# Kernel optimization log

Measured on AMD Instinct MI355X. Metric: run time of the kernel, lower is better.

The kernel has to match this reference:

```python
import jax, jax.numpy as jnp
import numpy as np

BSZ, IN_DIM, OUT_DIM = 512, 1024, 2048
M_AND = 5        # Anderson memory (self.m)
BETA = 1.0
LAM = 1e-4
ALPHA = 1.0
TOL = 1e-5
MAX_ITER = 50
M_MON = 1.0      # monotonicity parameter of MONSingleFc


def _multiply(A, B, z):
    # MONSingleFc.multiply: (1-m)z - z A^T A + z B^T - z B
    Az = z @ A.T
    return (1.0 - M_MON) * z - Az @ A + z @ B.T - z @ B


def _relu(z):
    return jnp.maximum(z, 0.0)


def _single_it(A, B, z, bias):
    zn = _multiply(A, B, z)
    zn = (1.0 - ALPHA) * z + ALPHA * (zn + bias)
    zn = _relu(zn)
    err = jnp.linalg.norm(zn - z) / (1e-6 + jnp.linalg.norm(zn))
    return zn, err


def _anderson_solve(A, B, bias):
    bsz, d = bias.shape
    dt = bias.dtype
    Z = jnp.zeros((bsz, M_AND, d), dt)
    F = jnp.zeros((bsz, M_AND, d), dt)
    z0 = jnp.zeros((bsz, d), dt)
    f0, _ = _single_it(A, B, z0, bias)
    F = F.at[:, 0].set(f0)
    Z = Z.at[:, 1].set(f0)
    f1, _ = _single_it(A, B, f0, bias)
    F = F.at[:, 1].set(f1)
    eye = jnp.eye(M_AND, dtype=dt)

    def cond(s):
        Z, F, it, err = s
        return (it < MAX_ITER) & (err > TOL)

    def body(s):
        Z, F, it, _ = s
        n = jnp.minimum(M_AND, it)
        mask = jnp.arange(M_AND) < n                         # active Anderson slots
        # For it < m the unused slots of Z and F are still zero, so G = F - Z
        # has zero rows there and GGt's Frobenius norm matches the :n slice.
        G = F - Z                                            # (bsz, m, d)
        GGt = jnp.einsum('bmd,bnd->bmn', G, G)
        nrm = jnp.linalg.norm(GGt.reshape(GGt.shape[0], -1), axis=-1)
        GGt = GGt / (nrm[:, None, None] + 1e-6)
        pair = mask[:, None] & mask[None, :]
        # identity padding on inactive slots keeps the solve well-posed and
        # yields alpha = 0 there, equivalent to slicing [:n+1, :n+1].
        Hb = jnp.where(pair, GGt + LAM * eye, eye)
        mk = mask.astype(dt)
        H = jnp.zeros((bsz, M_AND + 1, M_AND + 1), dt)
        H = H.at[:, 0, 1:].set(mk).at[:, 1:, 0].set(mk).at[:, 1:, 1:].set(Hb)
        y = jnp.zeros((bsz, M_AND + 1, 1), dt).at[:, 0, 0].set(1.0)
        alpha = jnp.linalg.solve(H, y)[:, 1:, 0]             # (bsz, m)
        z_new = BETA * jnp.einsum('bm,bmd->bd', alpha, F) \
              + (1.0 - BETA) * jnp.einsum('bm,bmd->bd', alpha, Z)
        slot = it % M_AND
        Z = Z.at[:, slot].set(z_new)
        zo, err = _single_it(A, B, z_new, bias)
        F = F.at[:, slot].set(zo)
        return Z, F, it + 1, err

    Z, F, it, err = jax.lax.while_loop(
        cond, body, (Z, F, jnp.array(2, jnp.int32), jnp.array(jnp.inf, dt)))
    slot = (it - 1) % M_AND
    return Z[:, slot]


def setup_inputs():
    key = jax.random.key(0)
    kx, ka, kb, kw, kub = jax.random.split(key, 5)
    s = 1.0 / np.sqrt(OUT_DIM).astype(np.float32)
    x = jax.random.normal(kx, (BSZ, IN_DIM), jnp.float32)
    # scaled so ||W|| < 1 -> forward-backward splitting converges (trained MON regime)
    A = 0.3 * s * jax.random.normal(ka, (OUT_DIM, OUT_DIM), jnp.float32)
    B = 0.1 * s * jax.random.normal(kb, (OUT_DIM, OUT_DIM), jnp.float32)
    U_W = (1.0 / np.sqrt(IN_DIM).astype(np.float32)) * jax.random.normal(kw, (OUT_DIM, IN_DIM), jnp.float32)
    U_b = 0.01 * jax.random.normal(kub, (OUT_DIM,), jnp.float32)
    return {"x": x, "A": A, "B": B, "U_W": U_W, "U_b": U_b}


def reference(x, A, B, U_W, U_b):
    bias = x @ U_W.T + U_b                       # linear_module.bias(x)
    z_star = _anderson_solve(A, B, bias)         # equilibrium (no-grad in torch)
    zn = _relu(_multiply(A, B, z_star) + bias)   # final full step: nonlin(linear(x, z*))
    return zn
```

## Files before the change

### kernel.cpp

```cpp
#include <hip/hip_runtime.h>
#include <hip/hip_bf16.h>
#include <math.h>

#define BSZ      512
#define IN_DIM   1024
#define OUT_DIM  2048
#define M_AND    5
#define LAM      1e-4f
#define TOL      1e-5f
#define MAX_ITER 50
#define SPLIT_IT 16
#define NBLK     256
#define ITERBLK  512

typedef __bf16 bf16x8 __attribute__((ext_vector_type(8)));
typedef float  f32x4  __attribute__((ext_vector_type(4)));
typedef unsigned short u16x8 __attribute__((ext_vector_type(8)));
typedef unsigned short u16x4 __attribute__((ext_vector_type(4)));
typedef __hip_bfloat16 bf16;

#define GAS __attribute__((address_space(1)))
#define LAS __attribute__((address_space(3)))

#define S_WAITCNT_VMCNT(N) asm volatile("s_waitcnt vmcnt(" #N ")" ::: "memory")

union BU { bf16 b; unsigned short u; };

__device__ __forceinline__ float bf2f(unsigned short u) {
    union { unsigned int i; float f; } c; c.i = (unsigned int)u << 16; return c.f;
}
__device__ __forceinline__ unsigned short f2bf(float f) {
    BU t; t.b = __float2bfloat16(f); return t.u;
}

static constexpr size_t BIAS_B = 0;
static constexpr size_t F_B    = BIAS_B + (size_t)BSZ * OUT_DIM * 4;
static constexpr size_t G_B    = F_B    + (size_t)BSZ * M_AND * OUT_DIM * 4;
static constexpr size_t ZH_B   = G_B    + (size_t)BSZ * M_AND * OUT_DIM * 2;
static constexpr size_t ZL_B   = ZH_B   + (size_t)BSZ * OUT_DIM * 2;
static constexpr size_t XH_B   = ZL_B   + (size_t)BSZ * OUT_DIM * 2;
static constexpr size_t XL_B   = XH_B   + (size_t)BSZ * IN_DIM * 2;
static constexpr size_t UH_B   = XL_B   + (size_t)BSZ * IN_DIM * 2;
static constexpr size_t UL_B   = UH_B   + (size_t)OUT_DIM * IN_DIM * 2;
static constexpr size_t AT_B   = UL_B   + (size_t)OUT_DIM * IN_DIM * 2;
static constexpr size_t WT_B   = AT_B   + (size_t)OUT_DIM * OUT_DIM * 2;
static constexpr size_t RED_B  = WT_B   + (size_t)OUT_DIM * OUT_DIM * 2;
static constexpr size_t BAR_B  = RED_B  + 512;
static constexpr size_t CTR_B  = BAR_B  + 64;
static constexpr size_t FLAG_B = CTR_B  + 256;
static constexpr size_t FSLOT_B = FLAG_B + 16;
static constexpr size_t CTRL_SZ = 512 + 64 + 256 + 16 + 16;

template<int ROUNDS>
__device__ __forceinline__ void stage_tile(const void* __restrict__ g0, int row_bytes,
                                           void* l0, int tid)
{
    #pragma unroll
    for (int q = 0; q < ROUNDS; ++q) {
        const int D   = q * 4096 + tid * 16;
        const int r   = D >> 7;
        const int cb  = D & 127;
        const int scb = cb ^ ((r & 7) << 4);
        const char* gsrc = (const char*)g0 + (size_t)r * row_bytes + scb;
        char* ldst = (char*)l0 + q * 4096 + (tid >> 6) * 1024;
        __builtin_amdgcn_global_load_lds((const GAS void*)gsrc, (LAS void*)ldst, 16, 0, 0);
    }
}

__device__ __forceinline__ bf16x8 read_frag(const void* tile, int row, int cb)
{
    return *(const bf16x8*)((const char*)tile + row * 128 + (cb ^ ((row & 7) << 4)));
}

__device__ __forceinline__ void gsync(unsigned int* bar)
{
    __syncthreads();
    if (threadIdx.x == 0) {
        __threadfence();
        const unsigned int g =
            __hip_atomic_load(&bar[1], __ATOMIC_ACQUIRE, __HIP_MEMORY_SCOPE_AGENT);
        const unsigned int a =
            __hip_atomic_fetch_add(&bar[0], 1u, __ATOMIC_ACQ_REL, __HIP_MEMORY_SCOPE_AGENT);
        if (a == NBLK - 1) {
            __hip_atomic_store(&bar[0], 0u, __ATOMIC_RELAXED, __HIP_MEMORY_SCOPE_AGENT);
            __hip_atomic_fetch_add(&bar[1], 1u, __ATOMIC_RELEASE, __HIP_MEMORY_SCOPE_AGENT);
        } else {
            while (__hip_atomic_load(&bar[1], __ATOMIC_ACQUIRE, __HIP_MEMORY_SCOPE_AGENT) == g)
                __builtin_amdgcn_s_sleep(1);
        }
        __threadfence();
    }
    __syncthreads();
}

__global__ __launch_bounds__(256)
void conv_hilo(const float* __restrict__ src, bf16* __restrict__ h, bf16* __restrict__ l)
{
    const size_t i4 = ((size_t)blockIdx.x * 256 + threadIdx.x) * 4;
    const float4 v = *(const float4*)&src[i4];
    const float vv[4] = {v.x, v.y, v.z, v.w};
    union { short4 s4; unsigned short u[4]; } ph, pl;
    #pragma unroll
    for (int j = 0; j < 4; ++j) {
        ph.u[j] = f2bf(vv[j]);
        pl.u[j] = f2bf(vv[j] - bf2f(ph.u[j]));
    }
    *(short4*)((char*)h + i4 * 2) = ph.s4;
    *(short4*)((char*)l + i4 * 2) = pl.s4;
}

__global__ __launch_bounds__(256)
void prep_at(const float* __restrict__ A, bf16* __restrict__ At)
{
    __shared__ float t[64][65];
    const int tid = threadIdx.x;
    const int k0 = blockIdx.y * 64, c0 = blockIdx.x * 64;
    const int cc = tid & 63, rr = tid >> 6;
    #pragma unroll
    for (int q = 0; q < 16; ++q)
        t[rr + 4 * q][cc] = A[(size_t)(k0 + rr + 4 * q) * OUT_DIM + c0 + cc];
    __syncthreads();
    #pragma unroll
    for (int q = 0; q < 16; ++q)
        At[(size_t)(c0 + rr + 4 * q) * OUT_DIM + k0 + cc] = __float2bfloat16(t[cc][rr + 4 * q]);
}

__global__ __launch_bounds__(256)
void w_mfma(const bf16* __restrict__ At, const float* __restrict__ Bm, bf16* __restrict__ Wt)
{
    __shared__ __align__(16) bf16 lds[2][2][64 * 64];
    const int tid = threadIdx.x;
    const int lane = tid & 63, wid = tid >> 6;
    const int wy = wid >> 1, wx = wid & 1;

    int bb = blockIdx.x;
    int ti = (int)((sqrtf(8.f * bb + 1.f) - 1.f) * 0.5f);
    while ((ti + 1) * (ti + 2) / 2 <= bb) ++ti;
    while (ti * (ti + 1) / 2 > bb) --ti;
    const int tj = bb - ti * (ti + 1) / 2;
    const int r0 = ti * 64, c0 = tj * 64;
    const bool diag = (ti == tj);

    f32x4 acc[2][2];
    #pragma unroll
    for (int i = 0; i < 2; ++i)
        #pragma unroll
        for (int j = 0; j < 2; ++j) acc[i][j] = 0;

    stage_tile<2>(At + (size_t)r0 * OUT_DIM, OUT_DIM * 2, lds[0][0], tid);
    stage_tile<2>(At + (size_t)c0 * OUT_DIM, OUT_DIM * 2, lds[0][1], tid);
    __syncthreads();
    int cur = 0;
    for (int t = 0; t < 32; ++t) {
        if (t + 1 < 32) {
            const int kk = (t + 1) * 64;
            stage_tile<2>(At + (size_t)r0 * OUT_DIM + kk, OUT_DIM * 2, lds[cur ^ 1][0], tid);
            stage_tile<2>(At + (size_t)c0 * OUT_DIM + kk, OUT_DIM * 2, lds[cur ^ 1][1], tid);
        }
        const bf16* Ta = lds[cur][0];
        const bf16* Tb = lds[cur][1];
        #pragma unroll
        for (int kf = 0; kf < 2; ++kf) {
            const int cb = kf * 64 + (lane >> 4) * 16;
            bf16x8 bfr[2];
            #pragma unroll
            for (int nj = 0; nj < 2; ++nj)
                bfr[nj] = read_frag(Tb, wx * 32 + nj * 16 + (lane & 15), cb);
            #pragma unroll
            for (int mi = 0; mi < 2; ++mi) {
                bf16x8 afr = read_frag(Ta, wy * 32 + mi * 16 + (lane & 15), cb);
                #pragma unroll
                for (int nj = 0; nj < 2; ++nj)
                    acc[mi][nj] = __builtin_amdgcn_mfma_f32_16x16x32_bf16(afr, bfr[nj], acc[mi][nj], 0, 0, 0);
            }
        }
        __syncthreads();
        cur ^= 1;
    }

    #pragma unroll
    for (int mi = 0; mi < 2; ++mi) {
        const int rb = r0 + wy * 32 + mi * 16 + (lane >> 4) * 4;
        #pragma unroll
        for (int nj = 0; nj < 2; ++nj) {
            const int c = c0 + wx * 32 + nj * 16 + (lane & 15);
            const float4 bc = *(const float4*)&Bm[(size_t)c * OUT_DIM + rb];
            const float bcv[4] = {bc.x, bc.y, bc.z, bc.w};
            union { short4 s4; unsigned short u[4]; } p;
            #pragma unroll
            for (int g = 0; g < 4; ++g) {
                const float a = acc[mi][nj][g];
                const float brc = Bm[(size_t)(rb + g) * OUT_DIM + c];
                const float w = bcv[g] - brc - a;
                p.u[g] = f2bf(w);
                if (!diag) {
                    const float wm = brc - bcv[g] - a;
                    *((unsigned short*)Wt + (size_t)(rb + g) * OUT_DIM + c) = f2bf(wm);
                }
            }
            *(short4*)((char*)Wt + ((size_t)c * OUT_DIM + rb) * 2) = p.s4;
        }
    }
}

__global__ __launch_bounds__(256)
void bias_mfma(const bf16* __restrict__ xh, const bf16* __restrict__ xl,
               const bf16* __restrict__ uh, const bf16* __restrict__ ul,
               const float* __restrict__ Ub, float* __restrict__ bias,
               float* __restrict__ F, unsigned short* __restrict__ G,
               unsigned short* __restrict__ zh, unsigned short* __restrict__ zl)
{
    __shared__ __align__(16) bf16 lds[2][4][64 * 64];
    const int tid = threadIdx.x;
    const int lane = tid & 63, wid = tid >> 6;
    const int wy = wid >> 1, wx = wid & 1;
    const int m0 = blockIdx.y * 64, n0 = blockIdx.x * 64;

    f32x4 acc[2][2];
    #pragma unroll
    for (int i = 0; i < 2; ++i)
        #pragma unroll
        for (int j = 0; j < 2; ++j) acc[i][j] = 0;

    stage_tile<2>(xh + (size_t)m0 * IN_DIM, IN_DIM * 2, lds[0][0], tid);
    stage_tile<2>(xl + (size_t)m0 * IN_DIM, IN_DIM * 2, lds[0][1], tid);
    stage_tile<2>(uh + (size_t)n0 * IN_DIM, IN_DIM * 2, lds[0][2], tid);
    stage_tile<2>(ul + (size_t)n0 * IN_DIM, IN_DIM * 2, lds[0][3], tid);
    __syncthreads();
    int cur = 0;
    for (int t = 0; t < 16; ++t) {
        if (t + 1 < 16) {
            const int kk = (t + 1) * 64;
            stage_tile<2>(xh + (size_t)m0 * IN_DIM + kk, IN_DIM * 2, lds[cur ^ 1][0], tid);
            stage_tile<2>(xl + (size_t)m0 * IN_DIM + kk, IN_DIM * 2, lds[cur ^ 1][1], tid);
            stage_tile<2>(uh + (size_t)n0 * IN_DIM + kk, IN_DIM * 2, lds[cur ^ 1][2], tid);
            stage_tile<2>(ul + (size_t)n0 * IN_DIM + kk, IN_DIM * 2, lds[cur ^ 1][3], tid);
        }
        const bf16* Txh = lds[cur][0];
        const bf16* Txl = lds[cur][1];
        const bf16* Tuh = lds[cur][2];
        const bf16* Tul = lds[cur][3];
        #pragma unroll
        for (int kf = 0; kf < 2; ++kf) {
            const int cb = kf * 64 + (lane >> 4) * 16;
            bf16x8 bh[2], bl[2];
            #pragma unroll
            for (int nj = 0; nj < 2; ++nj) {
                const int br = wx * 32 + nj * 16 + (lane & 15);
                bh[nj] = read_frag(Tuh, br, cb);
                bl[nj] = read_frag(Tul, br, cb);
            }
            #pragma unroll
            for (int mi = 0; mi < 2; ++mi) {
                const int ar = wy * 32 + mi * 16 + (lane & 15);
                bf16x8 ah = read_frag(Txh, ar, cb);
                bf16x8 al = read_frag(Txl, ar, cb);
                #pragma unroll
                for (int nj = 0; nj < 2; ++nj) {
                    acc[mi][nj] = __builtin_amdgcn_mfma_f32_16x16x32_bf16(ah, bh[nj], acc[mi][nj], 0, 0, 0);
                    acc[mi][nj] = __builtin_amdgcn_mfma_f32_16x16x32_bf16(ah, bl[nj], acc[mi][nj], 0, 0, 0);
                    acc[mi][nj] = __builtin_amdgcn_mfma_f32_16x16x32_bf16(al, bh[nj], acc[mi][nj], 0, 0, 0);
                }
            }
        }
        __syncthreads();
        cur ^= 1;
    }

    #pragma unroll
    for (int mi = 0; mi < 2; ++mi) {
        const int mb = m0 + wy * 32 + mi * 16 + (lane >> 4) * 4;
        #pragma unroll
        for (int nj = 0; nj < 2; ++nj) {
            const int n = n0 + wx * 32 + nj * 16 + (lane & 15);
            const float ub = Ub[n];
            #pragma unroll
            for (int g = 0; g < 4; ++g) {
                const int m = mb + g;
                const size_t idx = (size_t)m * OUT_DIM + n;
                const float v = acc[mi][nj][g] + ub;
                bias[idx] = v;
                const float f = fmaxf(v, 0.f);
                F[((size_t)m * M_AND + 0) * OUT_DIM + n] = f;
                G[((size_t)m * M_AND + 0) * OUT_DIM + n] = f2bf(f);
                const unsigned short h = f2bf(f);
                zh[idx] = h;
                zl[idx] = f2bf(f - bf2f(h));
            }
        }
    }
}

template<bool DO_ERR>
__device__ __forceinline__ void iter_core(
    const int m0, const int n0, const int tid,
    const unsigned short* __restrict__ zh, const unsigned short* __restrict__ zl,
    const bf16* __restrict__ Wt, const float* __restrict__ bias,
    float* __restrict__ F, unsigned short* __restrict__ G,
    float* red, bf16* lds_buf, const int slot, const int it)
{
    const int lane = tid & 63, wid = tid >> 6;
    const int wy = wid >> 1, wx = wid & 1;

    const int Dz  = tid * 16;
    const int zr  = Dz >> 7,  zcb  = Dz & 127;
    const size_t z_ro = (size_t)zr * 4096 + zcb;
    const int zo_l = zr * 128 + (zcb ^ ((zr & 7) << 4));
    const int Dw1 = 4096 + tid * 16;
    const int wr0 = Dz >> 7,  wcb0 = Dz & 127;
    const int wr1 = Dw1 >> 7, wcb1 = Dw1 & 127;
    const size_t w_ro0 = (size_t)wr0 * 4096 + wcb0;
    const size_t w_ro1 = (size_t)wr1 * 4096 + wcb1;
    const int wo_l0 = wr0 * 128 + (wcb0 ^ ((wr0 & 7) << 4));
    const int wo_l1 = wr1 * 128 + (wcb1 ^ ((wr1 & 7) << 4));

    const char* zbase = (const char*)zh + (size_t)m0 * 4096;
    const char* lbase = (const char*)zl + (size_t)m0 * 4096;
    const char* wbase = (const char*)Wt + (size_t)n0 * 4096;

    f32x4 acc[2];
    acc[0] = 0; acc[1] = 0;

    float4 rza, rla, rw0a, rw1a, rzb, rlb, rw0b, rw1b;

#define LOADR_(RZ, RL, RW0, RW1, KK)                                         \
    RZ  = *(const float4*)(zbase + (size_t)(KK) * 2 + z_ro);                 \
    RL  = *(const float4*)(lbase + (size_t)(KK) * 2 + z_ro);                 \
    RW0 = *(const float4*)(wbase + (size_t)(KK) * 2 + w_ro0);                \
    RW1 = *(const float4*)(wbase + (size_t)(KK) * 2 + w_ro1);

#define STEP_(T, RZ, RL, RW0, RW1, CUR)                                      \
  {                                                                          \
    if ((T) + 1 < 32) { S_WAITCNT_VMCNT(4); } else { S_WAITCNT_VMCNT(0); }   \
    __builtin_amdgcn_s_barrier();          \
    char* bp = (char*)lds_buf + (CUR) * 16384;                               \
    *(float4*)(bp + zo_l)         = RZ;                                      \
    *(float4*)(bp + 4096 + zo_l)  = RL;                                      \
    *(float4*)(bp + 8192 + wo_l0) = RW0;                                     \
    *(float4*)(bp + 8192 + wo_l1) = RW1;                                     \
    if ((T) + 2 < 32) { LOADR_(RZ, RL, RW0, RW1, ((T) + 2) * 64); }          \
    asm volatile("s_waitcnt lgkmcnt(0)" ::: "memory");                       \
    __builtin_amdgcn_sched_barrier(0);                                       \
    __builtin_amdgcn_s_barrier();         \
    __builtin_amdgcn_sched_barrier(0);                                       \
    __builtin_amdgcn_s_setprio(1);                                           \
    _Pragma("unroll")                                                        \
    for (int kf = 0; kf < 2; ++kf) {                                         \
        const int cb2 = kf * 64 + (lane >> 4) * 16;                          \
        bf16x8 b0  = read_frag(bp + 8192, wx * 32 + (lane & 15), cb2);       \
        bf16x8 b1  = read_frag(bp + 8192, wx * 32 + 16 + (lane & 15), cb2);  \
        bf16x8 ahv = read_frag(bp,        wy * 16 + (lane & 15), cb2);       \
        bf16x8 alv = read_frag(bp + 4096, wy * 16 + (lane & 15), cb2);       \
        acc[0] = __builtin_amdgcn_mfma_f32_16x16x32_bf16(ahv, b0, acc[0], 0, 0, 0); \
        acc[0] = __builtin_amdgcn_mfma_f32_16x16x32_bf16(alv, b0, acc[0], 0, 0, 0); \
        acc[1] = __builtin_amdgcn_mfma_f32_16x16x32_bf16(ahv, b1, acc[1], 0, 0, 0); \
        acc[1] = __builtin_amdgcn_mfma_f32_16x16x32_bf16(alv, b1, acc[1], 0, 0, 0); \
    }                                                                        \
    __builtin_amdgcn_s_setprio(0);                                           \
  }

    LOADR_(rza, rla, rw0a, rw1a, 0);
    LOADR_(rzb, rlb, rw0b, rw1b, 64);
    for (int tb = 0; tb < 16; ++tb) {
        const int t0 = 2 * tb;
        STEP_(t0,     rza, rla, rw0a, rw1a, 0);
        STEP_(t0 + 1, rzb, rlb, rw0b, rw1b, 1);
    }
#undef STEP_
#undef LOADR_

    float lnum = 0.f, lden = 0.f;
    const int mb = m0 + wy * 16 + (lane >> 4) * 4;
    #pragma unroll
    for (int nj = 0; nj < 2; ++nj) {
        const int n = n0 + wx * 32 + nj * 16 + (lane & 15);
        #pragma unroll
        for (int g = 0; g < 4; ++g) {
            const int m = mb + g;
            const size_t idx = (size_t)m * OUT_DIM + n;
            float v = acc[nj][g] + bias[idx];
            v = fmaxf(v, 0.f);
            const float zc = bf2f(zh[idx]) + bf2f(zl[idx]);
            const float gg = v - zc;
            F[((size_t)m * M_AND + slot) * OUT_DIM + n] = v;
            G[((size_t)m * M_AND + slot) * OUT_DIM + n] = f2bf(gg);
            if (DO_ERR) { lnum += gg * gg; lden += v * v; }
        }
    }

    if (DO_ERR) {
        #pragma unroll
        for (int off = 32; off; off >>= 1) {
            lnum += __shfl_down(lnum, off);
            lden += __shfl_down(lden, off);
        }
        __shared__ float swn[4], swd[4];
        if ((tid & 63) == 0) { swn[tid >> 6] = lnum; swd[tid >> 6] = lden; }
        __syncthreads();
        if (tid == 0) {
            atomicAdd(&red[2 * it],     swn[0] + swn[1] + swn[2] + swn[3]);
            atomicAdd(&red[2 * it + 1], swd[0] + swd[1] + swd[2] + swd[3]);
        }
    }
}

__device__ __forceinline__ void swz_mn(int bid, int& m0, int& n0)
{
    const int xcd = bid & 7, sl = bid >> 3;
    n0 = (xcd * 4 + (sl & 3)) * 64;
    m0 = (sl >> 2) * 32;
}

template<bool DO_ERR>
__global__ __launch_bounds__(256, 2)
void iter_mfma(const unsigned short* __restrict__ zh, const unsigned short* __restrict__ zl,
               const bf16* __restrict__ Wt, const float* __restrict__ bias,
               float* __restrict__ F, unsigned short* __restrict__ G,
               float* red, unsigned int* ctr, int* flag, int* fslot, int slot, int it)
{
    if (((volatile int*)flag)[0]) return;
    __shared__ __align__(16) bf16 lds_buf[2 * 8192];
    int m0, n0;
    swz_mn(blockIdx.x, m0, n0);
    iter_core<DO_ERR>(m0, n0, threadIdx.x, zh, zl, Wt, bias, F, G, red, lds_buf, slot, it);
    if (DO_ERR && threadIdx.x == 0) {
        __threadfence();
        const unsigned int done = atomicAdd(&ctr[it], 1u);
        if (done == ITERBLK - 1) {
            ((volatile int*)fslot)[0] = slot;
            const float num2 = ((volatile float*)red)[2 * it];
            const float den2 = ((volatile float*)red)[2 * it + 1];
            if (sqrtf(num2) <= TOL * (1e-6f + sqrtf(den2)))
                ((volatile int*)flag)[0] = 1;
        }
    }
}

__global__ __launch_bounds__(256)
void final_copy(const float* __restrict__ F, const int* __restrict__ fslot,
                float* __restrict__ out)
{
    const int s = ((volatile const int*)fslot)[0];
    const size_t i4 = ((size_t)blockIdx.x * 256 + threadIdx.x) * 4;
    const int m = (int)(i4 >> 11), n = (int)(i4 & 2047);
    *(float4*)&out[i4] = *(const float4*)&F[((size_t)m * M_AND + s) * OUT_DIM + n];
}

__global__ __launch_bounds__(512)
void anderson_kernel(const float* __restrict__ F, const unsigned short* __restrict__ G,
                     unsigned short* __restrict__ zh, unsigned short* __restrict__ zl,
                     int* flag, int it)
{
    if (((volatile int*)flag)[0]) return;
    const int b = blockIdx.x;
    const int tid = threadIdx.x;
    const int lane = tid & 63, wid = tid >> 6;
    const int n = (it < M_AND) ? it : M_AND;
    const int c0 = tid * 4;
    const unsigned short* Gb = G + (size_t)b * M_AND * OUT_DIM;
    const float* Fb = F + (size_t)b * M_AND * OUT_DIM;

    float g[M_AND][4];
    float4 f[M_AND];
    #pragma unroll
    for (int m = 0; m < M_AND; ++m) {
        f[m] = *(const float4*)(Fb + (size_t)m * OUT_DIM + c0);
        if (m < n) {
            const u16x4 gv = *(const u16x4*)(Gb + (size_t)m * OUT_DIM + c0);
            #pragma unroll
            for (int q = 0; q < 4; ++q) g[m][q] = bf2f(gv[q]);
        } else {
            #pragma unroll
            for (int q = 0; q < 4; ++q) g[m][q] = 0.f;
        }
    }

    float dots[15];
    {
        int p = 0;
        #pragma unroll
        for (int i = 0; i < M_AND; ++i)
            #pragma unroll
            for (int j = i; j < M_AND; ++j) {
                float s = 0.f;
                #pragma unroll
                for (int q = 0; q < 4; ++q) s += g[i][q] * g[j][q];
                dots[p++] = s;
            }
    }

    __shared__ float sred[15][8];
    #pragma unroll
    for (int p = 0; p < 15; ++p) {
        float v = dots[p];
        #pragma unroll
        for (int off = 32; off; off >>= 1) v += __shfl_xor(v, off);
        if (lane == 0) sred[p][wid] = v;
    }
    __syncthreads();

    __shared__ float s_alpha[M_AND];
    if (tid == 0) {
        float GGm[M_AND][M_AND];
        int p = 0;
        for (int i = 0; i < M_AND; ++i)
            for (int j = i; j < M_AND; ++j) {
                float v = 0.f;
                for (int w = 0; w < 8; ++w) v += sred[p][w];
                GGm[i][j] = v; GGm[j][i] = v; ++p;
            }
        float fro = 0.f;
        for (int i = 0; i < M_AND; ++i)
            for (int j = 0; j < M_AND; ++j) fro += GGm[i][j] * GGm[i][j];
        const float inv = 1.f / (sqrtf(fro) + 1e-6f);

        float Mm[M_AND][M_AND];
        for (int i = 0; i < n; ++i)
            for (int j = 0; j < n; ++j)
                Mm[i][j] = GGm[i][j] * inv + (i == j ? LAM : 0.f);

        float L[M_AND][M_AND];
        for (int i = 0; i < n; ++i)
            for (int j = 0; j <= i; ++j) {
                float s = Mm[i][j];
                for (int k = 0; k < j; ++k) s -= L[i][k] * L[j][k];
                L[i][j] = (i == j) ? sqrtf(fmaxf(s, 1e-20f)) : s / L[j][j];
            }
        float y[M_AND], u[M_AND];
        for (int i = 0; i < n; ++i) {
            float s = 1.f;
            for (int k = 0; k < i; ++k) s -= L[i][k] * y[k];
            y[i] = s / L[i][i];
        }
        for (int i = n - 1; i >= 0; --i) {
            float s = y[i];
            for (int k = i + 1; k < n; ++k) s -= L[k][i] * u[k];
            u[i] = s / L[i][i];
        }
        float su = 0.f;
        for (int i = 0; i < n; ++i) su += u[i];
        const float isu = 1.f / su;
        for (int m = 0; m < M_AND; ++m) s_alpha[m] = (m < n) ? u[m] * isu : 0.f;
    }
    __syncthreads();

    float z[4] = {};
    #pragma unroll
    for (int m = 0; m < M_AND; ++m) {
        if (m < n) {
            const float a = s_alpha[m];
            z[0] += a * f[m].x; z[1] += a * f[m].y;
            z[2] += a * f[m].z; z[3] += a * f[m].w;
        }
    }
    u16x4 hv, lv;
    #pragma unroll
    for (int q = 0; q < 4; ++q) {
        const unsigned short h = f2bf(z[q]);
        hv[q] = h;
        lv[q] = f2bf(z[q] - bf2f(h));
    }
    *(u16x4*)(zh + (size_t)b * OUT_DIM + c0) = hv;
    *(u16x4*)(zl + (size_t)b * OUT_DIM + c0) = lv;
}

__global__ __launch_bounds__(256)
void tail_loop(unsigned short* zh, unsigned short* zl,
               const bf16* __restrict__ Wt, const float* __restrict__ bias,
               float* F, unsigned short* G,
               float* red, unsigned int* bar, int* flag, int* fslot)
{
    if (((volatile int*)flag)[0]) return;
    __shared__ __align__(16) bf16 lds_buf[2 * 8192];
    __shared__ float sred2[2][2][15];
    __shared__ float s_alpha[2][M_AND];
    const int bid = blockIdx.x, tid = threadIdx.x;
    int m0a, n0a, m0b, n0b;
    swz_mn(bid, m0a, n0a);
    swz_mn(bid + 256, m0b, n0b);

    for (int it = SPLIT_IT; it < MAX_ITER; ++it) {
        {
            const int half = tid >> 7, lt = tid & 127;
            const int r = bid * 2 + half;
            const int wv = lt >> 6;
            const unsigned short* Gb = G + (size_t)r * M_AND * OUT_DIM;
            const float* Fb = F + (size_t)r * M_AND * OUT_DIM;
            const int c0 = lt * 16;

            float g[M_AND][16];
            #pragma unroll
            for (int m = 0; m < M_AND; ++m) {
                const u16x8 ga = *(const u16x8*)(Gb + (size_t)m * OUT_DIM + c0);
                const u16x8 gb2 = *(const u16x8*)(Gb + (size_t)m * OUT_DIM + c0 + 8);
                #pragma unroll
                for (int q = 0; q < 8; ++q) { g[m][q] = bf2f(ga[q]); g[m][8 + q] = bf2f(gb2[q]); }
            }
            {
                int p = 0;
                #pragma unroll
                for (int i = 0; i < M_AND; ++i)
                    #pragma unroll
                    for (int j = i; j < M_AND; ++j) {
                        float s = 0.f;
                        #pragma unroll
                        for (int q = 0; q < 16; ++q) s += g[i][q] * g[j][q];
                        float v = s;
                        #pragma unroll
                        for (int off = 32; off; off >>= 1) v += __shfl_xor(v, off);
                        if ((lt & 63) == 0) sred2[half][wv][p] = v;
                        ++p;
                    }
            }
            __syncthreads();
            if (lt == 0) {
                float GGm[M_AND][M_AND];
                int p = 0;
                for (int i = 0; i < M_AND; ++i)
                    for (int j = i; j < M_AND; ++j) {
                        const float v = sred2[half][0][p] + sred2[half][1][p];
                        GGm[i][j] = v; GGm[j][i] = v; ++p;
                    }
                float fro = 0.f;
                for (int i = 0; i < M_AND; ++i)
                    for (int j = 0; j < M_AND; ++j) fro += GGm[i][j] * GGm[i][j];
                const float inv = 1.f / (sqrtf(fro) + 1e-6f);
                float Mm[M_AND][M_AND];
                for (int i = 0; i < M_AND; ++i)
                    for (int j = 0; j < M_AND; ++j)
                        Mm[i][j] = GGm[i][j] * inv + (i == j ? LAM : 0.f);
                float L[M_AND][M_AND];
                for (int i = 0; i < M_AND; ++i)
                    for (int j = 0; j <= i; ++j) {
                        float s = Mm[i][j];
                        for (int k = 0; k < j; ++k) s -= L[i][k] * L[j][k];
                        L[i][j] = (i == j) ? sqrtf(fmaxf(s, 1e-20f)) : s / L[j][j];
                    }
                float y[M_AND], u[M_AND];
                for (int i = 0; i < M_AND; ++i) {
                    float s = 1.f;
                    for (int k = 0; k < i; ++k) s -= L[i][k] * y[k];
                    y[i] = s / L[i][i];
                }
                for (int i = M_AND - 1; i >= 0; --i) {
                    float s = y[i];
                    for (int k = i + 1; k < M_AND; ++k) s -= L[k][i] * u[k];
                    u[i] = s / L[i][i];
                }
                float su = 0.f;
                for (int i = 0; i < M_AND; ++i) su += u[i];
                const float isu = 1.f / su;
                for (int m = 0; m < M_AND; ++m) s_alpha[half][m] = u[m] * isu;
            }
            __syncthreads();
            float z[16] = {};
            for (int m = 0; m < M_AND; ++m) {
                const float a = s_alpha[half][m];
                #pragma unroll
                for (int q = 0; q < 4; ++q) {
                    const float4 fv = *(const float4*)(Fb + (size_t)m * OUT_DIM + c0 + q * 4);
                    z[q * 4 + 0] += a * fv.x; z[q * 4 + 1] += a * fv.y;
                    z[q * 4 + 2] += a * fv.z; z[q * 4 + 3] += a * fv.w;
                }
            }
            u16x8 hv[2], lv[2];
            #pragma unroll
            for (int q = 0; q < 16; ++q) {
                const unsigned short h = f2bf(z[q]);
                hv[q >> 3][q & 7] = h;
                lv[q >> 3][q & 7] = f2bf(z[q] - bf2f(h));
            }
            const size_t base = (size_t)r * OUT_DIM + c0;
            *(u16x8*)(zh + base)     = hv[0];
            *(u16x8*)(zh + base + 8) = hv[1];
            *(u16x8*)(zl + base)     = lv[0];
            *(u16x8*)(zl + base + 8) = lv[1];
        }
        gsync(bar);
        iter_core<true>(m0a, n0a, tid, zh, zl, Wt, bias, F, G, red, lds_buf, it % M_AND, it);
        __syncthreads();
        iter_core<true>(m0b, n0b, tid, zh, zl, Wt, bias, F, G, red, lds_buf, it % M_AND, it);
        gsync(bar);
        if (bid == 0 && tid == 0) ((volatile int*)fslot)[0] = it % M_AND;
        const float num2 = __hip_atomic_load(&red[2 * it], __ATOMIC_RELAXED, __HIP_MEMORY_SCOPE_AGENT);
        const float den2 = __hip_atomic_load(&red[2 * it + 1], __ATOMIC_RELAXED, __HIP_MEMORY_SCOPE_AGENT);
        if (sqrtf(num2) <= TOL * (1e-6f + sqrtf(den2))) break;
    }
}

extern "C" void kernel_launch(void* const* d_in, const int* in_sizes, int n_in,
                              void* d_out, int out_size, void* d_ws, size_t ws_size,
                              hipStream_t stream)
{
    const float* x  = (const float*)d_in[0];
    const float* A  = (const float*)d_in[1];
    const float* B  = (const float*)d_in[2];
    const float* UW = (const float*)d_in[3];
    const float* Ub = (const float*)d_in[4];
    float* out = (float*)d_out;
    char*  wsb = (char*)d_ws;

    float*          bias = (float*)(wsb + BIAS_B);
    float*          F    = (float*)(wsb + F_B);
    unsigned short* G    = (unsigned short*)(wsb + G_B);
    unsigned short* zh   = (unsigned short*)(wsb + ZH_B);
    unsigned short* zl   = (unsigned short*)(wsb + ZL_B);
    bf16*           xh   = (bf16*)(wsb + XH_B);
    bf16*           xl   = (bf16*)(wsb + XL_B);
    bf16*           uh   = (bf16*)(wsb + UH_B);
    bf16*           ul   = (bf16*)(wsb + UL_B);
    bf16*           At   = (bf16*)(wsb + AT_B);
    bf16*           Wt   = (bf16*)(wsb + WT_B);
    float*          red  = (float*)(wsb + RED_B);
    unsigned int*   bar  = (unsigned int*)(wsb + BAR_B);
    unsigned int*   ctr  = (unsigned int*)(wsb + CTR_B);
    int*            flag = (int*)(wsb + FLAG_B);
    int*            fslot= (int*)(wsb + FSLOT_B);

    hipMemsetAsync(wsb + RED_B, 0, CTRL_SZ, stream);

    conv_hilo<<<dim3(BSZ * IN_DIM / 1024),     256, 0, stream>>>(x,  xh, xl);
    conv_hilo<<<dim3(OUT_DIM * IN_DIM / 1024), 256, 0, stream>>>(UW, uh, ul);
    prep_at  <<<dim3(32, 32), 256, 0, stream>>>(A, At);
    w_mfma   <<<dim3(528), 256, 0, stream>>>(At, B, Wt);
    bias_mfma<<<dim3(32, 8), 256, 0, stream>>>(xh, xl, uh, ul, Ub, bias, F, G, zh, zl);

    iter_mfma<false><<<dim3(ITERBLK), 256, 0, stream>>>(zh, zl, Wt, bias, F, G,
                                                        red, ctr, flag, fslot, 1, 0);

    for (int it = 2; it < SPLIT_IT; ++it) {
        anderson_kernel<<<dim3(BSZ), 512, 0, stream>>>(F, G, zh, zl, flag, it);
        iter_mfma<true><<<dim3(ITERBLK), 256, 0, stream>>>(zh, zl, Wt, bias, F, G,
                                                           red, ctr, flag, fslot, it % M_AND, it);
    }
    tail_loop<<<dim3(NBLK), 256, 0, stream>>>(zh, zl, Wt, bias, F, G, red, bar, flag, fslot);
    final_copy<<<dim3(BSZ * OUT_DIM / 1024), 256, 0, stream>>>(F, fslot, out);
}
```

Measured before the change: 527.5 us.

## Fuse all Anderson iterations into one persistent 512-block kernel

The separate per-iteration anderson_kernel and iter_mfma launches for the first 16 iterations are removed. A single persistent kernel, solve_all, now runs with 512 blocks and grid barriers for every iteration. Each block handles one batch row's Anderson mixing and one GEMM tile per iteration, instead of the old tail loop's 256 blocks doing two tiles each. This removes about 28 kernel launches and the flag polling. In exchange it depends on all 512 blocks being co-resident, which launch_bounds(256,2) is meant to guarantee, and adds two grid barriers per iteration.

```diff
diff --git a/kernel.cpp b/kernel.cpp
--- a/kernel.cpp
+++ b/kernel.cpp
@@ -9,9 +9,7 @@
 #define LAM      1e-4f
 #define TOL      1e-5f
 #define MAX_ITER 50
-#define SPLIT_IT 16
-#define NBLK     256
-#define ITERBLK  512
+#define GS_N     512
 
 typedef __bf16 bf16x8 __attribute__((ext_vector_type(8)));
 typedef float  f32x4  __attribute__((ext_vector_type(4)));
@@ -46,10 +44,8 @@
 static constexpr size_t WT_B   = AT_B   + (size_t)OUT_DIM * OUT_DIM * 2;
 static constexpr size_t RED_B  = WT_B   + (size_t)OUT_DIM * OUT_DIM * 2;
 static constexpr size_t BAR_B  = RED_B  + 512;
-static constexpr size_t CTR_B  = BAR_B  + 64;
-static constexpr size_t FLAG_B = CTR_B  + 256;
-static constexpr size_t FSLOT_B = FLAG_B + 16;
-static constexpr size_t CTRL_SZ = 512 + 64 + 256 + 16 + 16;
+static constexpr size_t FSLOT_B = BAR_B + 64;
+static constexpr size_t CTRL_SZ = 512 + 64 + 16;
 
 template<int ROUNDS>
 __device__ __forceinline__ void stage_tile(const void* __restrict__ g0, int row_bytes,
@@ -81,7 +77,7 @@
             __hip_atomic_load(&bar[1], __ATOMIC_ACQUIRE, __HIP_MEMORY_SCOPE_AGENT);
         const unsigned int a =
             __hip_atomic_fetch_add(&bar[0], 1u, __ATOMIC_ACQ_REL, __HIP_MEMORY_SCOPE_AGENT);
-        if (a == NBLK - 1) {
+        if (a == GS_N - 1) {
             __hip_atomic_store(&bar[0], 0u, __ATOMIC_RELAXED, __HIP_MEMORY_SCOPE_AGENT);
             __hip_atomic_fetch_add(&bar[1], 1u, __ATOMIC_RELEASE, __HIP_MEMORY_SCOPE_AGENT);
         } else {
@@ -411,190 +407,41 @@
     m0 = (sl >> 2) * 32;
 }
 
-template<bool DO_ERR>
 __global__ __launch_bounds__(256, 2)
-void iter_mfma(const unsigned short* __restrict__ zh, const unsigned short* __restrict__ zl,
-               const bf16* __restrict__ Wt, const float* __restrict__ bias,
-               float* __restrict__ F, unsigned short* __restrict__ G,
-               float* red, unsigned int* ctr, int* flag, int* fslot, int slot, int it)
-{
-    if (((volatile int*)flag)[0]) return;
-    __shared__ __align__(16) bf16 lds_buf[2 * 8192];
-    int m0, n0;
-    swz_mn(blockIdx.x, m0, n0);
-    iter_core<DO_ERR>(m0, n0, threadIdx.x, zh, zl, Wt, bias, F, G, red, lds_buf, slot, it);
-    if (DO_ERR && threadIdx.x == 0) {
-        __threadfence();
-        const unsigned int done = atomicAdd(&ctr[it], 1u);
-        if (done == ITERBLK - 1) {
-            ((volatile int*)fslot)[0] = slot;
-            const float num2 = ((volatile float*)red)[2 * it];
-            const float den2 = ((volatile float*)red)[2 * it + 1];
-            if (sqrtf(num2) <= TOL * (1e-6f + sqrtf(den2)))
-                ((volatile int*)flag)[0] = 1;
-        }
-    }
-}
-
-__global__ __launch_bounds__(256)
-void final_copy(const float* __restrict__ F, const int* __restrict__ fslot,
-                float* __restrict__ out)
-{
-    const int s = ((volatile const int*)fslot)[0];
-    const size_t i4 = ((size_t)blockIdx.x * 256 + threadIdx.x) * 4;
-    const int m = (int)(i4 >> 11), n = (int)(i4 & 2047);
-    *(float4*)&out[i4] = *(const float4*)&F[((size_t)m * M_AND + s) * OUT_DIM + n];
-}
-
-__global__ __launch_bounds__(512)
-void anderson_kernel(const float* __restrict__ F, const unsigned short* __restrict__ G,
-                     unsigned short* __restrict__ zh, unsigned short* __restrict__ zl,
-                     int* flag, int it)
-{
-    if (((volatile int*)flag)[0]) return;
-    const int b = blockIdx.x;
-    const int tid = threadIdx.x;
-    const int lane = tid & 63, wid = tid >> 6;
-    const int n = (it < M_AND) ? it : M_AND;
-    const int c0 = tid * 4;
-    const unsigned short* Gb = G + (size_t)b * M_AND * OUT_DIM;
-    const float* Fb = F + (size_t)b * M_AND * OUT_DIM;
-
-    float g[M_AND][4];
-    float4 f[M_AND];
-    #pragma unroll
-    for (int m = 0; m < M_AND; ++m) {
-        f[m] = *(const float4*)(Fb + (size_t)m * OUT_DIM + c0);
-        if (m < n) {
-            const u16x4 gv = *(const u16x4*)(Gb + (size_t)m * OUT_DIM + c0);
-            #pragma unroll
-            for (int q = 0; q < 4; ++q) g[m][q] = bf2f(gv[q]);
-        } else {
-            #pragma unroll
-            for (int q = 0; q < 4; ++q) g[m][q] = 0.f;
-        }
-    }
-
-    float dots[15];
-    {
-        int p = 0;
-        #pragma unroll
-        for (int i = 0; i < M_AND; ++i)
-            #pragma unroll
-            for (int j = i; j < M_AND; ++j) {
-                float s = 0.f;
-                #pragma unroll
-                for (int q = 0; q < 4; ++q) s += g[i][q] * g[j][q];
-                dots[p++] = s;
-            }
-    }
-
-    __shared__ float sred[15][8];
-    #pragma unroll
-    for (int p = 0; p < 15; ++p) {
-        float v = dots[p];
-        #pragma unroll
-        for (int off = 32; off; off >>= 1) v += __shfl_xor(v, off);
-        if (lane == 0) sred[p][wid] = v;
-    }
-    __syncthreads();
-
-    __shared__ float s_alpha[M_AND];
-    if (tid == 0) {
-        float GGm[M_AND][M_AND];
-        int p = 0;
-        for (int i = 0; i < M_AND; ++i)
-            for (int j = i; j < M_AND; ++j) {
-                float v = 0.f;
-                for (int w = 0; w < 8; ++w) v += sred[p][w];
-                GGm[i][j] = v; GGm[j][i] = v; ++p;
-            }
-        float fro = 0.f;
-        for (int i = 0; i < M_AND; ++i)
-            for (int j = 0; j < M_AND; ++j) fro += GGm[i][j] * GGm[i][j];
-        const float inv = 1.f / (sqrtf(fro) + 1e-6f);
-
-        float Mm[M_AND][M_AND];
-        for (int i = 0; i < n; ++i)
-            for (int j = 0; j < n; ++j)
-                Mm[i][j] = GGm[i][j] * inv + (i == j ? LAM : 0.f);
-
-        float L[M_AND][M_AND];
-        for (int i = 0; i < n; ++i)
-            for (int j = 0; j <= i; ++j) {
-                float s = Mm[i][j];
-                for (int k = 0; k < j; ++k) s -= L[i][k] * L[j][k];
-                L[i][j] = (i == j) ? sqrtf(fmaxf(s, 1e-20f)) : s / L[j][j];
-            }
-        float y[M_AND], u[M_AND];
-        for (int i = 0; i < n; ++i) {
-            float s = 1.f;
-            for (int k = 0; k < i; ++k) s -= L[i][k] * y[k];
-            y[i] = s / L[i][i];
-        }
-        for (int i = n - 1; i >= 0; --i) {
-            float s = y[i];
-            for (int k = i + 1; k < n; ++k) s -= L[k][i] * u[k];
-            u[i] = s / L[i][i];
-        }
-        float su = 0.f;
-        for (int i = 0; i < n; ++i) su += u[i];
-        const float isu = 1.f / su;
-        for (int m = 0; m < M_AND; ++m) s_alpha[m] = (m < n) ? u[m] * isu : 0.f;
-    }
-    __syncthreads();
-
-    float z[4] = {};
-    #pragma unroll
-    for (int m = 0; m < M_AND; ++m) {
-        if (m < n) {
-            const float a = s_alpha[m];
-            z[0] += a * f[m].x; z[1] += a * f[m].y;
-            z[2] += a * f[m].z; z[3] += a * f[m].w;
-        }
-    }
-    u16x4 hv, lv;
-    #pragma unroll
-    for (int q = 0; q < 4; ++q) {
-        const unsigned short h = f2bf(z[q]);
-        hv[q] = h;
-        lv[q] = f2bf(z[q] - bf2f(h));
-    }
-    *(u16x4*)(zh + (size_t)b * OUT_DIM + c0) = hv;
-    *(u16x4*)(zl + (size_t)b * OUT_DIM + c0) = lv;
-}
-
-__global__ __launch_bounds__(256)
-void tail_loop(unsigned short* zh, unsigned short* zl,
+void solve_all(unsigned short* zh, unsigned short* zl,
                const bf16* __restrict__ Wt, const float* __restrict__ bias,
                float* F, unsigned short* G,
-               float* red, unsigned int* bar, int* flag, int* fslot)
-{
-    if (((volatile int*)flag)[0]) return;
+               float* red, unsigned int* bar, int* fslot)
+{
     __shared__ __align__(16) bf16 lds_buf[2 * 8192];
-    __shared__ float sred2[2][2][15];
-    __shared__ float s_alpha[2][M_AND];
+    __shared__ float sred[15][4];
+    __shared__ float s_alpha[M_AND];
     const int bid = blockIdx.x, tid = threadIdx.x;
-    int m0a, n0a, m0b, n0b;
-    swz_mn(bid, m0a, n0a);
-    swz_mn(bid + 256, m0b, n0b);
-
-    for (int it = SPLIT_IT; it < MAX_ITER; ++it) {
+    const int lane = tid & 63, wv = tid >> 6;
+    int m0, n0;
+    swz_mn(bid, m0, n0);
+
+    iter_core<false>(m0, n0, tid, zh, zl, Wt, bias, F, G, red, lds_buf, 1, 0);
+    gsync(bar);
+
+    for (int it = 2; it < MAX_ITER; ++it) {
         {
-            const int half = tid >> 7, lt = tid & 127;
-            const int r = bid * 2 + half;
-            const int wv = lt >> 6;
-            const unsigned short* Gb = G + (size_t)r * M_AND * OUT_DIM;
-            const float* Fb = F + (size_t)r * M_AND * OUT_DIM;
-            const int c0 = lt * 16;
-
-            float g[M_AND][16];
+            const int n = (it < M_AND) ? it : M_AND;
+            const unsigned short* Gb = G + (size_t)bid * M_AND * OUT_DIM;
+            const float* Fb = F + (size_t)bid * M_AND * OUT_DIM;
+            const int c0 = tid * 8;
+
+            float g[M_AND][8];
             #pragma unroll
             for (int m = 0; m < M_AND; ++m) {
-                const u16x8 ga = *(const u16x8*)(Gb + (size_t)m * OUT_DIM + c0);
-                const u16x8 gb2 = *(const u16x8*)(Gb + (size_t)m * OUT_DIM + c0 + 8);
-                #pragma unroll
-                for (int q = 0; q < 8; ++q) { g[m][q] = bf2f(ga[q]); g[m][8 + q] = bf2f(gb2[q]); }
+                if (m < n) {
+                    const u16x8 gvv = *(const u16x8*)(Gb + (size_t)m * OUT_DIM + c0);
+                    #pragma unroll
+                    for (int q = 0; q < 8; ++q) g[m][q] = bf2f(gvv[q]);
+                } else {
+                    #pragma unroll
+                    for (int q = 0; q < 8; ++q) g[m][q] = 0.f;
+                }
             }
             {
                 int p = 0;
@@ -604,88 +451,97 @@
                     for (int j = i; j < M_AND; ++j) {
                         float s = 0.f;
                         #pragma unroll
-                        for (int q = 0; q < 16; ++q) s += g[i][q] * g[j][q];
-                        float v = s;
+                        for (int q = 0; q < 8; ++q) s += g[i][q] * g[j][q];
                         #pragma unroll
-                        for (int off = 32; off; off >>= 1) v += __shfl_xor(v, off);
-                        if ((lt & 63) == 0) sred2[half][wv][p] = v;
+                        for (int off = 32; off; off >>= 1) s += __shfl_xor(s, off);
+                        if (lane == 0) sred[p][wv] = s;
                         ++p;
                     }
             }
             __syncthreads();
-            if (lt == 0) {
+            if (tid == 0) {
                 float GGm[M_AND][M_AND];
                 int p = 0;
                 for (int i = 0; i < M_AND; ++i)
                     for (int j = i; j < M_AND; ++j) {
-                        const float v = sred2[half][0][p] + sred2[half][1][p];
+                        const float v = sred[p][0] + sred[p][1] + sred[p][2] + sred[p][3];
                         GGm[i][j] = v; GGm[j][i] = v; ++p;
                     }
                 float fro = 0.f;
                 for (int i = 0; i < M_AND; ++i)
                     for (int j = 0; j < M_AND; ++j) fro += GGm[i][j] * GGm[i][j];
                 const float inv = 1.f / (sqrtf(fro) + 1e-6f);
+
                 float Mm[M_AND][M_AND];
-                for (int i = 0; i < M_AND; ++i)
-                    for (int j = 0; j < M_AND; ++j)
+                for (int i = 0; i < n; ++i)
+                    for (int j = 0; j < n; ++j)
                         Mm[i][j] = GGm[i][j] * inv + (i == j ? LAM : 0.f);
+
                 float L[M_AND][M_AND];
-                for (int i = 0; i < M_AND; ++i)
+                for (int i = 0; i < n; ++i)
                     for (int j = 0; j <= i; ++j) {
                         float s = Mm[i][j];
                         for (int k = 0; k < j; ++k) s -= L[i][k] * L[j][k];
                         L[i][j] = (i == j) ? sqrtf(fmaxf(s, 1e-20f)) : s / L[j][j];
                     }
                 float y[M_AND], u[M_AND];
-                for (int i = 0; i < M_AND; ++i) {
+                for (int i = 0; i < n; ++i) {
                     float s = 1.f;
                     for (int k = 0; k < i; ++k) s -= L[i][k] * y[k];
                     y[i] = s / L[i][i];
                 }
-                for (int i = M_AND - 1; i >= 0; --i) {
+                for (int i = n - 1; i >= 0; --i) {
                     float s = y[i];
-                    for (int k = i + 1; k < M_AND; ++k) s -= L[k][i] * u[k];
+                    for (int k = i + 1; k < n; ++k) s -= L[k][i] * u[k];
                     u[i] = s / L[i][i];
                 }
                 float su = 0.f;
-                for (int i = 0; i < M_AND; ++i) su += u[i];
+                for (int i = 0; i < n; ++i) su += u[i];
                 const float isu = 1.f / su;
-                for (int m = 0; m < M_AND; ++m) s_alpha[half][m] = u[m] * isu;
+                for (int m = 0; m < M_AND; ++m) s_alpha[m] = (m < n) ? u[m] * isu : 0.f;
             }
             __syncthreads();
-            float z[16] = {};
+
+            float zv[8] = {};
             for (int m = 0; m < M_AND; ++m) {
-                const float a = s_alpha[half][m];
-                #pragma unroll
-                for (int q = 0; q < 4; ++q) {
-                    const float4 fv = *(const float4*)(Fb + (size_t)m * OUT_DIM + c0 + q * 4);
-                    z[q * 4 + 0] += a * fv.x; z[q * 4 + 1] += a * fv.y;
-                    z[q * 4 + 2] += a * fv.z; z[q * 4 + 3] += a * fv.w;
+                if (m < n) {
+                    const float a = s_alpha[m];
+                    const float4 fa  = *(const float4*)(Fb + (size_t)m * OUT_DIM + c0);
+                    const float4 fb2 = *(const float4*)(Fb + (size_t)m * OUT_DIM + c0 + 4);
+                    zv[0] += a * fa.x;  zv[1] += a * fa.y;  zv[2] += a * fa.z;  zv[3] += a * fa.w;
+                    zv[4] += a * fb2.x; zv[5] += a * fb2.y; zv[6] += a * fb2.z; zv[7] += a * fb2.w;
                 }
             }
-            u16x8 hv[2], lv[2];
-            #pragma unroll
-            for (int q = 0; q < 16; ++q) {
-                const unsigned short h = f2bf(z[q]);
-                hv[q >> 3][q & 7] = h;
-                lv[q >> 3][q & 7] = f2bf(z[q] - bf2f(h));
-            }
-            const size_t base = (size_t)r * OUT_DIM + c0;
-            *(u16x8*)(zh + base)     = hv[0];
-            *(u16x8*)(zh + base + 8) = hv[1];
-            *(u16x8*)(zl + base)     = lv[0];
-            *(u16x8*)(zl + base + 8) = lv[1];
+            u16x8 hv, lv;
+            #pragma unroll
+            for (int q = 0; q < 8; ++q) {
+                const unsigned short h = f2bf(zv[q]);
+                hv[q] = h;
+                lv[q] = f2bf(zv[q] - bf2f(h));
+            }
+            *(u16x8*)(zh + (size_t)bid * OUT_DIM + c0) = hv;
+            *(u16x8*)(zl + (size_t)bid * OUT_DIM + c0) = lv;
         }
         gsync(bar);
-        iter_core<true>(m0a, n0a, tid, zh, zl, Wt, bias, F, G, red, lds_buf, it % M_AND, it);
-        __syncthreads();
-        iter_core<true>(m0b, n0b, tid, zh, zl, Wt, bias, F, G, red, lds_buf, it % M_AND, it);
+
+        iter_core<true>(m0, n0, tid, zh, zl, Wt, bias, F, G, red, lds_buf, it % M_AND, it);
         gsync(bar);
+
         if (bid == 0 && tid == 0) ((volatile int*)fslot)[0] = it % M_AND;
         const float num2 = __hip_atomic_load(&red[2 * it], __ATOMIC_RELAXED, __HIP_MEMORY_SCOPE_AGENT);
         const float den2 = __hip_atomic_load(&red[2 * it + 1], __ATOMIC_RELAXED, __HIP_MEMORY_SCOPE_AGENT);
         if (sqrtf(num2) <= TOL * (1e-6f + sqrtf(den2))) break;
     }
+}
+
+__global__ __launch_bounds__(256)
+void final_copy(const float* __restrict__ F, const int* __restrict__ fslot,
+                float* __restrict__ out)
+{
+    const int s = ((volatile const int*)fslot)[0];
+    const size_t i4 = ((size_t)blockIdx.x * 256 + threadIdx.x) * 4;
+    const int m = (int)(i4 >> 11), n = (int)(i4 & 2047);
+    *(float4*)&out[i4] = *(const float4*)&F[((size_t)m * M_AND + s) * OUT_DIM + n];
 }
 
 extern "C" void kernel_launch(void* const* d_in, const int* in_sizes, int n_in,
@@ -713,8 +569,6 @@
     bf16*           Wt   = (bf16*)(wsb + WT_B);
     float*          red  = (float*)(wsb + RED_B);
     unsigned int*   bar  = (unsigned int*)(wsb + BAR_B);
-    unsigned int*   ctr  = (unsigned int*)(wsb + CTR_B);
-    int*            flag = (int*)(wsb + FLAG_B);
     int*            fslot= (int*)(wsb + FSLOT_B);
 
     hipMemsetAsync(wsb + RED_B, 0, CTRL_SZ, stream);
@@ -725,14 +579,7 @@
     w_mfma   <<<dim3(528), 256, 0, stream>>>(At, B, Wt);
     bias_mfma<<<dim3(32, 8), 256, 0, stream>>>(xh, xl, uh, ul, Ub, bias, F, G, zh, zl);
 
-    iter_mfma<false><<<dim3(ITERBLK), 256, 0, stream>>>(zh, zl, Wt, bias, F, G,
-                                                        red, ctr, flag, fslot, 1, 0);
-
-    for (int it = 2; it < SPLIT_IT; ++it) {
-        anderson_kernel<<<dim3(BSZ), 512, 0, stream>>>(F, G, zh, zl, flag, it);
-        iter_mfma<true><<<dim3(ITERBLK), 256, 0, stream>>>(zh, zl, Wt, bias, F, G,
-                                                           red, ctr, flag, fslot, it % M_AND, it);
-    }
-    tail_loop<<<dim3(NBLK), 256, 0, stream>>>(zh, zl, Wt, bias, F, G, red, bar, flag, fslot);
+    solve_all<<<dim3(GS_N), 256, 0, stream>>>(zh, zl, Wt, bias, F, G, red, bar, fslot);
+
     final_copy<<<dim3(BSZ * OUT_DIM / 1024), 256, 0, stream>>>(F, fslot, out);
 }
```

New measurement: 1.675 ms. +217.6%, slower.
